# Optimization experiments

Hardware: AMD Instinct MI355X
Metric: run time of the kernel (lower is better)

Reference implementation:

```python
import jax, jax.numpy as jnp
import numpy as np

B, DIM, F, H = 16384, 64, 8, 8
D2 = DIM // 2


def setup_inputs() -> dict:
    key = jax.random.key(0)
    ks = jax.random.split(key, 8)
    s = 0.1  # small init so exp(s_net) stays well-conditioned
    return {
        "x": jax.random.normal(ks[0], (B, DIM), jnp.float32),
        "x_star": jax.random.normal(ks[1], (B, DIM), jnp.float32),
        "W0": jax.random.normal(ks[2], (F, 4, H, D2), jnp.float32) * s,
        "b0": jax.random.normal(ks[3], (F, 4, H), jnp.float32) * s,
        "W1": jax.random.normal(ks[4], (F, 4, H, H), jnp.float32) * s,
        "b1": jax.random.normal(ks[5], (F, 4, H), jnp.float32) * s,
        "W2": jax.random.normal(ks[6], (F, 4, D2, H), jnp.float32) * s,
        "b2": jax.random.normal(ks[7], (F, 4, D2), jnp.float32) * s,
    }


def _fcnn(v, w0, c0, w1, c1, w2, c2):
    # FCNN: Linear -> Tanh -> Linear -> Tanh -> Linear, on a single vector v [D2]
    h = jnp.tanh(w0 @ v + c0)
    h = jnp.tanh(w1 @ h + c1)
    return w2 @ h + c2


def _phi(v, params):
    # Chain of n_flows RealNVP coupling layers on a single sample v [DIM].
    def step(v, p):
        W0, b0, W1, b1, W2, b2 = p  # leading axis 4 = (t1, s1, t2, s2)
        lo, up = v[:D2], v[D2:]
        t1 = _fcnn(lo, W0[0], b0[0], W1[0], b1[0], W2[0], b2[0])
        s1 = _fcnn(lo, W0[1], b0[1], W1[1], b1[1], W2[1], b2[1])
        up = t1 + up * jnp.exp(s1)
        t2 = _fcnn(up, W0[2], b0[2], W1[2], b1[2], W2[2], b2[2])
        s2 = _fcnn(up, W0[3], b0[3], W1[3], b1[3], W2[3], b2[3])
        lo = t2 + lo * jnp.exp(s2)
        return jnp.concatenate([lo, up]), None

    z, _ = jax.lax.scan(step, v, params)
    return z


def reference(x, x_star, W0, b0, W1, b1, W2, b2):
    params = (W0, b0, W1, b1, W2, b2)
    # Per-sample Jacobian of the flow (replaces torch autograd loop): [B, DIM, DIM]
    jac = jax.vmap(jax.jacfwd(lambda v: _phi(v, params)))(x)
    # -grad of quadratic potential (feature=None): -2 * (x - x_star)
    g = -2.0 * (x - x_star)
    # torch.solve(potential_grad, phi_jac): solve J u = g per sample
    return jnp.linalg.solve(jac, g[..., None])[..., 0]
```

## Files before the change

### kernel.cpp

```cpp
#include <hip/hip_runtime.h>


namespace {

typedef __fp16 f16x2 __attribute__((ext_vector_type(2)));
typedef __fp16 v4h __attribute__((ext_vector_type(4)));
typedef __fp16 v8h __attribute__((ext_vector_type(8)));
typedef float f32x4 __attribute__((ext_vector_type(4)));
typedef unsigned int u32;
typedef u32 u32x2 __attribute__((ext_vector_type(2)));
typedef u32 u32x4 __attribute__((ext_vector_type(4)));

constexpr int NB = 16384;

__device__ __forceinline__ float frcp(float x) { return __builtin_amdgcn_rcpf(x); }
__device__ __forceinline__ float ftanh(float x) {
  float e = __expf(2.f * x);
  return 1.f - 2.f * frcp(e + 1.f);
}
__device__ __forceinline__ f16x2 pk(float a, float b) {
  return __builtin_amdgcn_cvt_pkrtz(a, b);
}
__device__ __forceinline__ v8h mk8(f16x2 a, f16x2 b, f16x2 c, f16x2 d) {
  const u32x4 t = {__builtin_bit_cast(u32, a), __builtin_bit_cast(u32, b),
                   __builtin_bit_cast(u32, c), __builtin_bit_cast(u32, d)};
  return __builtin_bit_cast(v8h, t);
}
__device__ __forceinline__ v4h mk4(f16x2 a, f16x2 b) {
  const u32x2 t = {__builtin_bit_cast(u32, a), __builtin_bit_cast(u32, b)};
  return __builtin_bit_cast(v4h, t);
}

__device__ __forceinline__ int pbase(int p) {
  return ((p >> 1) << 2) + ((p & 1) << 1);
}

}

#define L3_FWD(P, BB, D0, D1, D2, D3)                                         \
  do {                                                                        \
    const bool act_ = ((BB) < 2) == (q < 2);                                  \
    v4h Ab = *(const v4h*)(LW2 + ((P)*256 + (BB)*64 + abbase));               \
    Ab = act_ ? Ab : z4;                                                      \
    const f32x4 cb = *(const f32x4*)(LB2 + ((P)*4 + (BB)) * 16 + q * 4);      \
    const f32x4 ob =                                                          \
        __builtin_amdgcn_mfma_f32_16x16x16f16(Ab, H2v, cb, 0, 0, 0);          \
    D0 = ob[0]; D1 = ob[1]; D2 = ob[2]; D3 = ob[3];                           \
  } while (0)

#define FWD_UPD(J, W) W##J = fmaf(W##J, __expf(s##J), t##J)

#define FWD_HALF(P, V, W)                                                     \
  do {                                                                        \
    const v8h Bq = mk8(pk(V##0, V##1), pk(V##2, V##3), pk(V##4, V##5),        \
                       pk(V##6, V##7));                                       \
    const v8h A0 = *(const v8h*)(LW0 + (((P)*64 + q * 16 + n) << 2));         \
    const f32x4 c0 = *(const f32x4*)(LB0 + (P)*16 + q * 4);                   \
    f32x4 d1 = __builtin_amdgcn_mfma_f32_16x16x32_f16(A0, Bq, c0, 0, 0, 0);   \
    const f16x2 H1a = pk(ftanh(d1[0]), ftanh(d1[1]));                         \
    const f16x2 H1b = pk(ftanh(d1[2]), ftanh(d1[3]));                         \
    v4h A1 = *(const v4h*)(LW1 + ((P)*64 + a1off));                           \
    A1 = act1 ? A1 : z4;                                                      \
    const f32x4 c1 = *(const f32x4*)(LB1 + (P)*16 + q * 4);                   \
    f32x4 d2 =                                                                \
        __builtin_amdgcn_mfma_f32_16x16x16f16(A1, mk4(H1a, H1b), c1, 0, 0, 0);\
    const f16x2 H2a = pk(ftanh(d2[0]), ftanh(d2[1]));                         \
    const f16x2 H2b = pk(ftanh(d2[2]), ftanh(d2[3]));                         \
    const v4h H2v = mk4(H2a, H2b);                                            \
    float t0, t1, t2, t3, t4, t5, t6, t7;                                     \
    float s0, s1, s2, s3, s4, s5, s6, s7;                                     \
    L3_FWD(P, 0, t0, t1, t2, t3);                                             \
    L3_FWD(P, 1, t4, t5, t6, t7);                                             \
    L3_FWD(P, 2, s0, s1, s2, s3);                                             \
    L3_FWD(P, 3, s4, s5, s6, s7);                                             \
    FWD_UPD(0, W); FWD_UPD(1, W); FWD_UPD(2, W); FWD_UPD(3, W);               \
    FWD_UPD(4, W); FWD_UPD(5, W); FWD_UPD(6, W); FWD_UPD(7, W);               \
  } while (0)

#define L3_BWD(P, BB, D0, D1, D2, D3, J0, J1, J2, J3)                         \
  do {                                                                        \
    const bool act_ = ((BB) < 2) == (q < 2);                                  \
    v4h Ab = *(const v4h*)(LW2 + ((P)*256 + (BB)*64 + abbase));               \
    Ab = act_ ? Ab : z4;                                                      \
    const f32x4 cb = *(const f32x4*)(LB2 + ((P)*4 + (BB)) * 16 + q * 4);      \
    const f32x4 ob =                                                          \
        __builtin_amdgcn_mfma_f32_16x16x16f16(Ab, H2v, cb, 0, 0, 0);          \
    const f32x4 jb =                                                          \
        __builtin_amdgcn_mfma_f32_16x16x16f16(Ab, G2v, zc, 0, 0, 0);          \
    D0 = ob[0]; D1 = ob[1]; D2 = ob[2]; D3 = ob[3];                           \
    J0 = jb[0]; J1 = jb[1]; J2 = jb[2]; J3 = jb[3];                           \
  } while (0)

#define BWD_INV(J, ST, DME)                                                   \
  do {                                                                        \
    const float esi_ = __expf(-s##J);                                         \
    const float dd_ = ST##J - t##J;                                           \
    ST##J = dd_ * esi_;                                                       \
    DME##J = (DME##J - ut##J - dd_ * us##J) * esi_;                           \
  } while (0)

#define BWD_HALF(P, ST, DME, DOT, VIN)                                        \
  do {                                                                        \
    const v8h Bv = mk8(pk(VIN##0, VIN##1), pk(VIN##2, VIN##3),                \
                       pk(VIN##4, VIN##5), pk(VIN##6, VIN##7));               \
    const v8h Bu = mk8(pk(DOT##0, DOT##1), pk(DOT##2, DOT##3),                \
                       pk(DOT##4, DOT##5), pk(DOT##6, DOT##7));               \
    const v8h A0 = *(const v8h*)(LW0 + (((P)*64 + q * 16 + n) << 2));         \
    const f32x4 c0 = *(const f32x4*)(LB0 + (P)*16 + q * 4);                   \
    f32x4 d1 = __builtin_amdgcn_mfma_f32_16x16x32_f16(A0, Bv, c0, 0, 0, 0);   \
    f32x4 d1u = __builtin_amdgcn_mfma_f32_16x16x32_f16(A0, Bu, zc, 0, 0, 0);  \
    const float h10 = ftanh(d1[0]), h11 = ftanh(d1[1]);                       \
    const float h12 = ftanh(d1[2]), h13 = ftanh(d1[3]);                       \
    const f16x2 H1a = pk(h10, h11);                                           \
    const f16x2 H1b = pk(h12, h13);                                           \
    const f16x2 G1a =                                                         \
        pk((1.f - h10 * h10) * d1u[0], (1.f - h11 * h11) * d1u[1]);           \
    const f16x2 G1b =                                                         \
        pk((1.f - h12 * h12) * d1u[2], (1.f - h13 * h13) * d1u[3]);           \
    v4h A1 = *(const v4h*)(LW1 + ((P)*64 + a1off));                           \
    A1 = act1 ? A1 : z4;                                                      \
    const f32x4 c1 = *(const f32x4*)(LB1 + (P)*16 + q * 4);                   \
    f32x4 d2 =                                                                \
        __builtin_amdgcn_mfma_f32_16x16x16f16(A1, mk4(H1a, H1b), c1, 0, 0, 0);\
    f32x4 d2u =                                                               \
        __builtin_amdgcn_mfma_f32_16x16x16f16(A1, mk4(G1a, G1b), zc, 0, 0, 0);\
    const float h20 = ftanh(d2[0]), h21 = ftanh(d2[1]);                       \
    const float h22 = ftanh(d2[2]), h23 = ftanh(d2[3]);                       \
    const f16x2 G2a =                                                         \
        pk((1.f - h20 * h20) * d2u[0], (1.f - h21 * h21) * d2u[1]);           \
    const f16x2 G2b =                                                         \
        pk((1.f - h22 * h22) * d2u[2], (1.f - h23 * h23) * d2u[3]);           \
    const v4h H2v = mk4(pk(h20, h21), pk(h22, h23));                          \
    const v4h G2v = mk4(G2a, G2b);                                            \
    float t0, t1, t2, t3, t4, t5, t6, t7;                                     \
    float s0, s1, s2, s3, s4, s5, s6, s7;                                     \
    float ut0, ut1, ut2, ut3, ut4, ut5, ut6, ut7;                             \
    float us0, us1, us2, us3, us4, us5, us6, us7;                             \
    L3_BWD(P, 0, t0, t1, t2, t3, ut0, ut1, ut2, ut3);                         \
    L3_BWD(P, 1, t4, t5, t6, t7, ut4, ut5, ut6, ut7);                         \
    L3_BWD(P, 2, s0, s1, s2, s3, us0, us1, us2, us3);                         \
    L3_BWD(P, 3, s4, s5, s6, s7, us4, us5, us6, us7);                         \
    BWD_INV(0, ST, DME); BWD_INV(1, ST, DME);                                 \
    BWD_INV(2, ST, DME); BWD_INV(3, ST, DME);                                 \
    BWD_INV(4, ST, DME); BWD_INV(5, ST, DME);                                 \
    BWD_INV(6, ST, DME); BWD_INV(7, ST, DME);                                 \
  } while (0)

__global__ __attribute__((amdgpu_flat_work_group_size(512, 512),
                          amdgpu_waves_per_eu(4, 8))) void nf_policy_kernel(
    const float* __restrict__ x, const float* __restrict__ xs,
    const float* __restrict__ gW0, const float* __restrict__ gb0,
    const float* __restrict__ gW1, const float* __restrict__ gb1,
    const float* __restrict__ gW2, const float* __restrict__ gb2,
    float* __restrict__ out) {
  __shared__ __align__(16) f16x2 LW0[4096];
  __shared__ __align__(16) f16x2 LW1[1024];
  __shared__ __align__(16) f16x2 LW2[4096];
  __shared__ __align__(16) float LB0[256];
  __shared__ __align__(16) float LB1[256];
  __shared__ __align__(16) float LB2[1024];

  const int tid = threadIdx.x;
  for (int i = tid; i < 4096; i += 512) {
    const int p = i >> 8, rem = i & 255, qq = rem >> 6, rem2 = rem & 63;
    const int mm = rem2 >> 2, w = rem2 & 3;
    const int net = pbase(p) + (mm >> 3);
    const int h = mm & 7, k0 = qq * 8 + w * 2;
    const float* src = gW0 + net * 256 + h * 32 + k0;
    LW0[i] = pk(src[0], src[1]);
  }
  for (int i = tid; i < 1024; i += 512) {
    const int p = i >> 6, rem = i & 63, half = rem >> 5;
    const int row = (rem >> 2) & 7, kk = rem & 3;
    const int net = pbase(p) + half;
    const float* src = gW1 + net * 64 + row * 8 + kk * 2;
    LW1[i] = pk(src[0], src[1]);
  }
  for (int i = tid; i < 4096; i += 512) {
    const int p = i >> 8, rem = i & 255, b = rem >> 6, rem2 = rem & 63;
    const int mm = rem2 >> 2, kk = rem2 & 3;
    const int net = pbase(p) + (b >> 1);
    const int d = 8 * (mm >> 2) + ((b & 1) << 2) + (mm & 3);
    const float* src = gW2 + net * 256 + d * 8 + kk * 2;
    LW2[i] = pk(src[0], src[1]);
  }
  for (int i = tid; i < 256; i += 512) {
    const int p = i >> 4, mm = i & 15;
    const int net = pbase(p) + (mm >> 3);
    LB0[i] = gb0[net * 8 + (mm & 7)];
    LB1[i] = gb1[net * 8 + (mm & 7)];
  }
  for (int i = tid; i < 1024; i += 512) {
    const int p = i >> 6, b = (i >> 4) & 3, mm = i & 15;
    const int net = pbase(p) + (b >> 1);
    const int d = 8 * (mm >> 2) + ((b & 1) << 2) + (mm & 3);
    LB2[i] = gb2[net * 32 + d];
  }
  __syncthreads();

  const int lane = tid & 63;
  const int wv = tid >> 6;
  const int n = lane & 15;
  const int q = lane >> 4;
  const int e = blockIdx.x * 32 + wv * 4 + (n & 3);

  const v4h z4 = {(__fp16)0.f, (__fp16)0.f, (__fp16)0.f, (__fp16)0.f};
  const f32x4 zc = {0.f, 0.f, 0.f, 0.f};
  const bool act1 = (n < 8) == (q < 2);
  const int a1off = ((n & 7) << 2) + ((q & 1) << 1) + ((n >= 8) ? 32 : 0);
  const int abbase = n * 4 + ((q & 1) << 1);

  float lo0, lo1, lo2, lo3, lo4, lo5, lo6, lo7;
  float up0, up1, up2, up3, up4, up5, up6, up7;
  float av0, av1, av2, av3, av4, av5, av6, av7;
  float bv0, bv1, bv2, bv3, bv4, bv5, bv6, bv7;
  {
    const float* xe = x + (size_t)e * 64;
    const float* se = xs + (size_t)e * 64;
    const float4 a0 = *(const float4*)(xe + q * 8);
    const float4 a1 = *(const float4*)(xe + q * 8 + 4);
    const float4 u0 = *(const float4*)(xe + 32 + q * 8);
    const float4 u1 = *(const float4*)(xe + 32 + q * 8 + 4);
    const float4 p0 = *(const float4*)(se + q * 8);
    const float4 p1 = *(const float4*)(se + q * 8 + 4);
    const float4 r0 = *(const float4*)(se + 32 + q * 8);
    const float4 r1 = *(const float4*)(se + 32 + q * 8 + 4);
    lo0 = a0.x; lo1 = a0.y; lo2 = a0.z; lo3 = a0.w;
    lo4 = a1.x; lo5 = a1.y; lo6 = a1.z; lo7 = a1.w;
    up0 = u0.x; up1 = u0.y; up2 = u0.z; up3 = u0.w;
    up4 = u1.x; up5 = u1.y; up6 = u1.z; up7 = u1.w;
    av0 = -2.f * (a0.x - p0.x); av1 = -2.f * (a0.y - p0.y);
    av2 = -2.f * (a0.z - p0.z); av3 = -2.f * (a0.w - p0.w);
    av4 = -2.f * (a1.x - p1.x); av5 = -2.f * (a1.y - p1.y);
    av6 = -2.f * (a1.z - p1.z); av7 = -2.f * (a1.w - p1.w);
    bv0 = -2.f * (u0.x - r0.x); bv1 = -2.f * (u0.y - r0.y);
    bv2 = -2.f * (u0.z - r0.z); bv3 = -2.f * (u0.w - r0.w);
    bv4 = -2.f * (u1.x - r1.x); bv5 = -2.f * (u1.y - r1.y);
    bv6 = -2.f * (u1.z - r1.z); bv7 = -2.f * (u1.w - r1.w);
  }

#pragma clang loop unroll(disable)
  for (int st = 0; st < 8; ++st) {
    const int p0i = 2 * st;
    FWD_HALF(p0i, lo, up);
    FWD_HALF(p0i + 1, up, lo);
  }

#pragma clang loop unroll(disable)
  for (int st = 7; st >= 0; --st) {
    const int p0i = 2 * st;
    BWD_HALF(p0i + 1, lo, av, bv, up);
    BWD_HALF(p0i, up, bv, av, lo);
  }

  if (n < 4) {
    float* oe = out + (size_t)e * 64;
    float4 v;
    v.x = av0; v.y = av1; v.z = av2; v.w = av3;
    *(float4*)(oe + q * 8) = v;
    v.x = av4; v.y = av5; v.z = av6; v.w = av7;
    *(float4*)(oe + q * 8 + 4) = v;
    v.x = bv0; v.y = bv1; v.z = bv2; v.w = bv3;
    *(float4*)(oe + 32 + q * 8) = v;
    v.x = bv4; v.y = bv5; v.z = bv6; v.w = bv7;
    *(float4*)(oe + 32 + q * 8 + 4) = v;
  }
}

extern "C" void kernel_launch(void* const* d_in, const int* in_sizes, int n_in,
                              void* d_out, int out_size, void* d_ws,
                              size_t ws_size, hipStream_t stream) {
  const float* x  = (const float*)d_in[0];
  const float* xs = (const float*)d_in[1];
  const float* W0 = (const float*)d_in[2];
  const float* b0 = (const float*)d_in[3];
  const float* W1 = (const float*)d_in[4];
  const float* b1 = (const float*)d_in[5];
  const float* W2 = (const float*)d_in[6];
  const float* b2 = (const float*)d_in[7];
  float* out = (float*)d_out;

  dim3 grid(NB / 32);
  dim3 block(512);
  nf_policy_kernel<<<grid, block, 0, stream>>>(x, xs, W0, b0, W1, b1, W2, b2,
                                               out);
}
```

Measured before the change: 108.8 us.

## Give each MFMA column its own sample and interleave two sample groups per wave

Before, each wave handled only 4 samples, with each sample copied across 4 MFMA column groups (n&3), so most of the MFMA N dimension held duplicate work. Now each of the 16 columns carries a distinct sample, and each wave processes two 16-sample groups (a and b), whose independent MFMAs are interleaved to hide latency. Blocks shrink to 128 threads covering 64 samples, with waves_per_eu lowered to 1-2 to make room for the doubled register state. Redundant compute drops by roughly 4x per sample, but register pressure rises and occupancy falls, with some risk of spills.

```diff
diff --git a/kernel.cpp b/kernel.cpp
--- a/kernel.cpp
+++ b/kernel.cpp
@@ -37,117 +37,160 @@
 
 }
 
-#define L3_FWD(P, BB, D0, D1, D2, D3)                                         \
+#define MFMA32(A, B, C) __builtin_amdgcn_mfma_f32_16x16x32_f16(A, B, C, 0, 0, 0)
+#define MFMA16(A, B, C) __builtin_amdgcn_mfma_f32_16x16x16f16(A, B, C, 0, 0, 0)
+
+#define L3_FWD2(P, BB, DA0, DA1, DA2, DA3, DB0, DB1, DB2, DB3)                \
   do {                                                                        \
     const bool act_ = ((BB) < 2) == (q < 2);                                  \
     v4h Ab = *(const v4h*)(LW2 + ((P)*256 + (BB)*64 + abbase));               \
     Ab = act_ ? Ab : z4;                                                      \
     const f32x4 cb = *(const f32x4*)(LB2 + ((P)*4 + (BB)) * 16 + q * 4);      \
-    const f32x4 ob =                                                          \
-        __builtin_amdgcn_mfma_f32_16x16x16f16(Ab, H2v, cb, 0, 0, 0);          \
-    D0 = ob[0]; D1 = ob[1]; D2 = ob[2]; D3 = ob[3];                           \
-  } while (0)
-
-#define FWD_UPD(J, W) W##J = fmaf(W##J, __expf(s##J), t##J)
-
-#define FWD_HALF(P, V, W)                                                     \
-  do {                                                                        \
-    const v8h Bq = mk8(pk(V##0, V##1), pk(V##2, V##3), pk(V##4, V##5),        \
-                       pk(V##6, V##7));                                       \
+    const f32x4 oa = MFMA16(Ab, H2va, cb);                                    \
+    const f32x4 ob = MFMA16(Ab, H2vb, cb);                                    \
+    DA0 = oa[0]; DA1 = oa[1]; DA2 = oa[2]; DA3 = oa[3];                       \
+    DB0 = ob[0]; DB1 = ob[1]; DB2 = ob[2]; DB3 = ob[3];                       \
+  } while (0)
+
+#define FWD_UPD(S, J, W) W##S##J = fmaf(W##S##J, __expf(s##S##J), t##S##J)
+
+#define FWD_HALF2(P, V, W)                                                    \
+  do {                                                                        \
+    const v8h Bqa = mk8(pk(V##a0, V##a1), pk(V##a2, V##a3),                   \
+                        pk(V##a4, V##a5), pk(V##a6, V##a7));                  \
+    const v8h Bqb = mk8(pk(V##b0, V##b1), pk(V##b2, V##b3),                   \
+                        pk(V##b4, V##b5), pk(V##b6, V##b7));                  \
     const v8h A0 = *(const v8h*)(LW0 + (((P)*64 + q * 16 + n) << 2));         \
     const f32x4 c0 = *(const f32x4*)(LB0 + (P)*16 + q * 4);                   \
-    f32x4 d1 = __builtin_amdgcn_mfma_f32_16x16x32_f16(A0, Bq, c0, 0, 0, 0);   \
-    const f16x2 H1a = pk(ftanh(d1[0]), ftanh(d1[1]));                         \
-    const f16x2 H1b = pk(ftanh(d1[2]), ftanh(d1[3]));                         \
+    f32x4 d1a = MFMA32(A0, Bqa, c0);                                          \
+    f32x4 d1b = MFMA32(A0, Bqb, c0);                                          \
+    const f16x2 H1aa = pk(ftanh(d1a[0]), ftanh(d1a[1]));                      \
+    const f16x2 H1ab = pk(ftanh(d1a[2]), ftanh(d1a[3]));                      \
+    const f16x2 H1ba = pk(ftanh(d1b[0]), ftanh(d1b[1]));                      \
+    const f16x2 H1bb = pk(ftanh(d1b[2]), ftanh(d1b[3]));                      \
     v4h A1 = *(const v4h*)(LW1 + ((P)*64 + a1off));                           \
     A1 = act1 ? A1 : z4;                                                      \
     const f32x4 c1 = *(const f32x4*)(LB1 + (P)*16 + q * 4);                   \
-    f32x4 d2 =                                                                \
-        __builtin_amdgcn_mfma_f32_16x16x16f16(A1, mk4(H1a, H1b), c1, 0, 0, 0);\
-    const f16x2 H2a = pk(ftanh(d2[0]), ftanh(d2[1]));                         \
-    const f16x2 H2b = pk(ftanh(d2[2]), ftanh(d2[3]));                         \
-    const v4h H2v = mk4(H2a, H2b);                                            \
-    float t0, t1, t2, t3, t4, t5, t6, t7;                                     \
-    float s0, s1, s2, s3, s4, s5, s6, s7;                                     \
-    L3_FWD(P, 0, t0, t1, t2, t3);                                             \
-    L3_FWD(P, 1, t4, t5, t6, t7);                                             \
-    L3_FWD(P, 2, s0, s1, s2, s3);                                             \
-    L3_FWD(P, 3, s4, s5, s6, s7);                                             \
-    FWD_UPD(0, W); FWD_UPD(1, W); FWD_UPD(2, W); FWD_UPD(3, W);               \
-    FWD_UPD(4, W); FWD_UPD(5, W); FWD_UPD(6, W); FWD_UPD(7, W);               \
-  } while (0)
-
-#define L3_BWD(P, BB, D0, D1, D2, D3, J0, J1, J2, J3)                         \
+    f32x4 d2a = MFMA16(A1, mk4(H1aa, H1ab), c1);                              \
+    f32x4 d2b = MFMA16(A1, mk4(H1ba, H1bb), c1);                              \
+    const v4h H2va = mk4(pk(ftanh(d2a[0]), ftanh(d2a[1])),                    \
+                         pk(ftanh(d2a[2]), ftanh(d2a[3])));                   \
+    const v4h H2vb = mk4(pk(ftanh(d2b[0]), ftanh(d2b[1])),                    \
+                         pk(ftanh(d2b[2]), ftanh(d2b[3])));                   \
+    float ta0, ta1, ta2, ta3, ta4, ta5, ta6, ta7;                             \
+    float sa0, sa1, sa2, sa3, sa4, sa5, sa6, sa7;                             \
+    float tb0, tb1, tb2, tb3, tb4, tb5, tb6, tb7;                             \
+    float sb0, sb1, sb2, sb3, sb4, sb5, sb6, sb7;                             \
+    L3_FWD2(P, 0, ta0, ta1, ta2, ta3, tb0, tb1, tb2, tb3);                    \
+    L3_FWD2(P, 1, ta4, ta5, ta6, ta7, tb4, tb5, tb6, tb7);                    \
+    L3_FWD2(P, 2, sa0, sa1, sa2, sa3, sb0, sb1, sb2, sb3);                    \
+    L3_FWD2(P, 3, sa4, sa5, sa6, sa7, sb4, sb5, sb6, sb7);                    \
+    FWD_UPD(a, 0, W); FWD_UPD(a, 1, W); FWD_UPD(a, 2, W); FWD_UPD(a, 3, W);   \
+    FWD_UPD(a, 4, W); FWD_UPD(a, 5, W); FWD_UPD(a, 6, W); FWD_UPD(a, 7, W);   \
+    FWD_UPD(b, 0, W); FWD_UPD(b, 1, W); FWD_UPD(b, 2, W); FWD_UPD(b, 3, W);   \
+    FWD_UPD(b, 4, W); FWD_UPD(b, 5, W); FWD_UPD(b, 6, W); FWD_UPD(b, 7, W);   \
+  } while (0)
+
+#define L3_BWD2(P, BB, DA0, DA1, DA2, DA3, JA0, JA1, JA2, JA3,                \
+                DB0, DB1, DB2, DB3, JB0, JB1, JB2, JB3)                       \
   do {                                                                        \
     const bool act_ = ((BB) < 2) == (q < 2);                                  \
     v4h Ab = *(const v4h*)(LW2 + ((P)*256 + (BB)*64 + abbase));               \
     Ab = act_ ? Ab : z4;                                                      \
     const f32x4 cb = *(const f32x4*)(LB2 + ((P)*4 + (BB)) * 16 + q * 4);      \
-    const f32x4 ob =                                                          \
-        __builtin_amdgcn_mfma_f32_16x16x16f16(Ab, H2v, cb, 0, 0, 0);          \
-    const f32x4 jb =                                                          \
-        __builtin_amdgcn_mfma_f32_16x16x16f16(Ab, G2v, zc, 0, 0, 0);          \
-    D0 = ob[0]; D1 = ob[1]; D2 = ob[2]; D3 = ob[3];                           \
-    J0 = jb[0]; J1 = jb[1]; J2 = jb[2]; J3 = jb[3];                           \
-  } while (0)
-
-#define BWD_INV(J, ST, DME)                                                   \
-  do {                                                                        \
-    const float esi_ = __expf(-s##J);                                         \
-    const float dd_ = ST##J - t##J;                                           \
-    ST##J = dd_ * esi_;                                                       \
-    DME##J = (DME##J - ut##J - dd_ * us##J) * esi_;                           \
-  } while (0)
-
-#define BWD_HALF(P, ST, DME, DOT, VIN)                                        \
-  do {                                                                        \
-    const v8h Bv = mk8(pk(VIN##0, VIN##1), pk(VIN##2, VIN##3),                \
-                       pk(VIN##4, VIN##5), pk(VIN##6, VIN##7));               \
-    const v8h Bu = mk8(pk(DOT##0, DOT##1), pk(DOT##2, DOT##3),                \
-                       pk(DOT##4, DOT##5), pk(DOT##6, DOT##7));               \
+    const f32x4 oa = MFMA16(Ab, H2va, cb);                                    \
+    const f32x4 ja = MFMA16(Ab, G2va, zc);                                    \
+    const f32x4 ob = MFMA16(Ab, H2vb, cb);                                    \
+    const f32x4 jb = MFMA16(Ab, G2vb, zc);                                    \
+    DA0 = oa[0]; DA1 = oa[1]; DA2 = oa[2]; DA3 = oa[3];                       \
+    JA0 = ja[0]; JA1 = ja[1]; JA2 = ja[2]; JA3 = ja[3];                       \
+    DB0 = ob[0]; DB1 = ob[1]; DB2 = ob[2]; DB3 = ob[3];                       \
+    JB0 = jb[0]; JB1 = jb[1]; JB2 = jb[2]; JB3 = jb[3];                       \
+  } while (0)
+
+#define BWD_INV(S, J, ST, DME)                                                \
+  do {                                                                        \
+    const float esi_ = __expf(-s##S##J);                                      \
+    const float dd_ = ST##S##J - t##S##J;                                     \
+    ST##S##J = dd_ * esi_;                                                    \
+    DME##S##J = (DME##S##J - ut##S##J - dd_ * us##S##J) * esi_;               \
+  } while (0)
+
+#define BWD_HALF2(P, ST, DME, DOT, VIN)                                       \
+  do {                                                                        \
+    const v8h Bva = mk8(pk(VIN##a0, VIN##a1), pk(VIN##a2, VIN##a3),           \
+                        pk(VIN##a4, VIN##a5), pk(VIN##a6, VIN##a7));          \
+    const v8h Bua = mk8(pk(DOT##a0, DOT##a1), pk(DOT##a2, DOT##a3),           \
+                        pk(DOT##a4, DOT##a5), pk(DOT##a6, DOT##a7));          \
+    const v8h Bvb = mk8(pk(VIN##b0, VIN##b1), pk(VIN##b2, VIN##b3),           \
+                        pk(VIN##b4, VIN##b5), pk(VIN##b6, VIN##b7));          \
+    const v8h Bub = mk8(pk(DOT##b0, DOT##b1), pk(DOT##b2, DOT##b3),           \
+                        pk(DOT##b4, DOT##b5), pk(DOT##b6, DOT##b7));          \
     const v8h A0 = *(const v8h*)(LW0 + (((P)*64 + q * 16 + n) << 2));         \
     const f32x4 c0 = *(const f32x4*)(LB0 + (P)*16 + q * 4);                   \
-    f32x4 d1 = __builtin_amdgcn_mfma_f32_16x16x32_f16(A0, Bv, c0, 0, 0, 0);   \
-    f32x4 d1u = __builtin_amdgcn_mfma_f32_16x16x32_f16(A0, Bu, zc, 0, 0, 0);  \
-    const float h10 = ftanh(d1[0]), h11 = ftanh(d1[1]);                       \
-    const float h12 = ftanh(d1[2]), h13 = ftanh(d1[3]);                       \
-    const f16x2 H1a = pk(h10, h11);                                           \
-    const f16x2 H1b = pk(h12, h13);                                           \
-    const f16x2 G1a =                                                         \
-        pk((1.f - h10 * h10) * d1u[0], (1.f - h11 * h11) * d1u[1]);           \
-    const f16x2 G1b =                                                         \
-        pk((1.f - h12 * h12) * d1u[2], (1.f - h13 * h13) * d1u[3]);           \
+    f32x4 d1a = MFMA32(A0, Bva, c0);                                          \
+    f32x4 d1ua = MFMA32(A0, Bua, zc);                                         \
+    f32x4 d1b = MFMA32(A0, Bvb, c0);                                          \
+    f32x4 d1ub = MFMA32(A0, Bub, zc);                                         \
+    const float h10a = ftanh(d1a[0]), h11a = ftanh(d1a[1]);                   \
+    const float h12a = ftanh(d1a[2]), h13a = ftanh(d1a[3]);                   \
+    const float h10b = ftanh(d1b[0]), h11b = ftanh(d1b[1]);                   \
+    const float h12b = ftanh(d1b[2]), h13b = ftanh(d1b[3]);                   \
+    const f16x2 G1aa =                                                        \
+        pk((1.f - h10a * h10a) * d1ua[0], (1.f - h11a * h11a) * d1ua[1]);     \
+    const f16x2 G1ab =                                                        \
+        pk((1.f - h12a * h12a) * d1ua[2], (1.f - h13a * h13a) * d1ua[3]);     \
+    const f16x2 G1ba =                                                        \
+        pk((1.f - h10b * h10b) * d1ub[0], (1.f - h11b * h11b) * d1ub[1]);     \
+    const f16x2 G1bb =                                                        \
+        pk((1.f - h12b * h12b) * d1ub[2], (1.f - h13b * h13b) * d1ub[3]);     \
     v4h A1 = *(const v4h*)(LW1 + ((P)*64 + a1off));                           \
     A1 = act1 ? A1 : z4;                                                      \
     const f32x4 c1 = *(const f32x4*)(LB1 + (P)*16 + q * 4);                   \
-    f32x4 d2 =                                                                \
-        __builtin_amdgcn_mfma_f32_16x16x16f16(A1, mk4(H1a, H1b), c1, 0, 0, 0);\
-    f32x4 d2u =                                                               \
-        __builtin_amdgcn_mfma_f32_16x16x16f16(A1, mk4(G1a, G1b), zc, 0, 0, 0);\
-    const float h20 = ftanh(d2[0]), h21 = ftanh(d2[1]);                       \
-    const float h22 = ftanh(d2[2]), h23 = ftanh(d2[3]);                       \
-    const f16x2 G2a =                                                         \
-        pk((1.f - h20 * h20) * d2u[0], (1.f - h21 * h21) * d2u[1]);           \
-    const f16x2 G2b =                                                         \
-        pk((1.f - h22 * h22) * d2u[2], (1.f - h23 * h23) * d2u[3]);           \
-    const v4h H2v = mk4(pk(h20, h21), pk(h22, h23));                          \
-    const v4h G2v = mk4(G2a, G2b);                                            \
-    float t0, t1, t2, t3, t4, t5, t6, t7;                                     \
-    float s0, s1, s2, s3, s4, s5, s6, s7;                                     \
-    float ut0, ut1, ut2, ut3, ut4, ut5, ut6, ut7;                             \
-    float us0, us1, us2, us3, us4, us5, us6, us7;                             \
-    L3_BWD(P, 0, t0, t1, t2, t3, ut0, ut1, ut2, ut3);                         \
-    L3_BWD(P, 1, t4, t5, t6, t7, ut4, ut5, ut6, ut7);                         \
-    L3_BWD(P, 2, s0, s1, s2, s3, us0, us1, us2, us3);                         \
-    L3_BWD(P, 3, s4, s5, s6, s7, us4, us5, us6, us7);                         \
-    BWD_INV(0, ST, DME); BWD_INV(1, ST, DME);                                 \
-    BWD_INV(2, ST, DME); BWD_INV(3, ST, DME);                                 \
-    BWD_INV(4, ST, DME); BWD_INV(5, ST, DME);                                 \
-    BWD_INV(6, ST, DME); BWD_INV(7, ST, DME);                                 \
-  } while (0)
-
-__global__ __attribute__((amdgpu_flat_work_group_size(512, 512),
-                          amdgpu_waves_per_eu(4, 8))) void nf_policy_kernel(
+    f32x4 d2a = MFMA16(A1, mk4(pk(h10a, h11a), pk(h12a, h13a)), c1);          \
+    f32x4 d2ua = MFMA16(A1, mk4(G1aa, G1ab), zc);                             \
+    f32x4 d2b = MFMA16(A1, mk4(pk(h10b, h11b), pk(h12b, h13b)), c1);          \
+    f32x4 d2ub = MFMA16(A1, mk4(G1ba, G1bb), zc);                             \
+    const float h20a = ftanh(d2a[0]), h21a = ftanh(d2a[1]);                   \
+    const float h22a = ftanh(d2a[2]), h23a = ftanh(d2a[3]);                   \
+    const float h20b = ftanh(d2b[0]), h21b = ftanh(d2b[1]);                   \
+    const float h22b = ftanh(d2b[2]), h23b = ftanh(d2b[3]);                   \
+    const v4h H2va = mk4(pk(h20a, h21a), pk(h22a, h23a));                     \
+    const v4h H2vb = mk4(pk(h20b, h21b), pk(h22b, h23b));                     \
+    const v4h G2va =                                                          \
+        mk4(pk((1.f - h20a * h20a) * d2ua[0], (1.f - h21a * h21a) * d2ua[1]), \
+            pk((1.f - h22a * h22a) * d2ua[2], (1.f - h23a * h23a) * d2ua[3]));\
+    const v4h G2vb =                                                          \
+        mk4(pk((1.f - h20b * h20b) * d2ub[0], (1.f - h21b * h21b) * d2ub[1]), \
+            pk((1.f - h22b * h22b) * d2ub[2], (1.f - h23b * h23b) * d2ub[3]));\
+    float ta0, ta1, ta2, ta3, ta4, ta5, ta6, ta7;                             \
+    float sa0, sa1, sa2, sa3, sa4, sa5, sa6, sa7;                             \
+    float uta0, uta1, uta2, uta3, uta4, uta5, uta6, uta7;                     \
+    float usa0, usa1, usa2, usa3, usa4, usa5, usa6, usa7;                     \
+    float tb0, tb1, tb2, tb3, tb4, tb5, tb6, tb7;                             \
+    float sb0, sb1, sb2, sb3, sb4, sb5, sb6, sb7;                             \
+    float utb0, utb1, utb2, utb3, utb4, utb5, utb6, utb7;                     \
+    float usb0, usb1, usb2, usb3, usb4, usb5, usb6, usb7;                     \
+    L3_BWD2(P, 0, ta0, ta1, ta2, ta3, uta0, uta1, uta2, uta3,                 \
+            tb0, tb1, tb2, tb3, utb0, utb1, utb2, utb3);                      \
+    L3_BWD2(P, 1, ta4, ta5, ta6, ta7, uta4, uta5, uta6, uta7,                 \
+            tb4, tb5, tb6, tb7, utb4, utb5, utb6, utb7);                      \
+    L3_BWD2(P, 2, sa0, sa1, sa2, sa3, usa0, usa1, usa2, usa3,                 \
+            sb0, sb1, sb2, sb3, usb0, usb1, usb2, usb3);                      \
+    L3_BWD2(P, 3, sa4, sa5, sa6, sa7, usa4, usa5, usa6, usa7,                 \
+            sb4, sb5, sb6, sb7, usb4, usb5, usb6, usb7);                      \
+    BWD_INV(a, 0, ST, DME); BWD_INV(a, 1, ST, DME);                           \
+    BWD_INV(a, 2, ST, DME); BWD_INV(a, 3, ST, DME);                           \
+    BWD_INV(a, 4, ST, DME); BWD_INV(a, 5, ST, DME);                           \
+    BWD_INV(a, 6, ST, DME); BWD_INV(a, 7, ST, DME);                           \
+    BWD_INV(b, 0, ST, DME); BWD_INV(b, 1, ST, DME);                           \
+    BWD_INV(b, 2, ST, DME); BWD_INV(b, 3, ST, DME);                           \
+    BWD_INV(b, 4, ST, DME); BWD_INV(b, 5, ST, DME);                           \
+    BWD_INV(b, 6, ST, DME); BWD_INV(b, 7, ST, DME);                           \
+  } while (0)
+
+__global__ __attribute__((amdgpu_flat_work_group_size(128, 128),
+                          amdgpu_waves_per_eu(1, 2))) void nf_policy_kernel(
     const float* __restrict__ x, const float* __restrict__ xs,
     const float* __restrict__ gW0, const float* __restrict__ gb0,
     const float* __restrict__ gW1, const float* __restrict__ gb1,
@@ -161,7 +204,7 @@
   __shared__ __align__(16) float LB2[1024];
 
   const int tid = threadIdx.x;
-  for (int i = tid; i < 4096; i += 512) {
+  for (int i = tid; i < 4096; i += 128) {
     const int p = i >> 8, rem = i & 255, qq = rem >> 6, rem2 = rem & 63;
     const int mm = rem2 >> 2, w = rem2 & 3;
     const int net = pbase(p) + (mm >> 3);
@@ -169,14 +212,14 @@
     const float* src = gW0 + net * 256 + h * 32 + k0;
     LW0[i] = pk(src[0], src[1]);
   }
-  for (int i = tid; i < 1024; i += 512) {
+  for (int i = tid; i < 1024; i += 128) {
     const int p = i >> 6, rem = i & 63, half = rem >> 5;
     const int row = (rem >> 2) & 7, kk = rem & 3;
     const int net = pbase(p) + half;
     const float* src = gW1 + net * 64 + row * 8 + kk * 2;
     LW1[i] = pk(src[0], src[1]);
   }
-  for (int i = tid; i < 4096; i += 512) {
+  for (int i = tid; i < 4096; i += 128) {
     const int p = i >> 8, rem = i & 255, b = rem >> 6, rem2 = rem & 63;
     const int mm = rem2 >> 2, kk = rem2 & 3;
     const int net = pbase(p) + (b >> 1);
@@ -184,13 +227,13 @@
     const float* src = gW2 + net * 256 + d * 8 + kk * 2;
     LW2[i] = pk(src[0], src[1]);
   }
-  for (int i = tid; i < 256; i += 512) {
+  for (int i = tid; i < 256; i += 128) {
     const int p = i >> 4, mm = i & 15;
     const int net = pbase(p) + (mm >> 3);
     LB0[i] = gb0[net * 8 + (mm & 7)];
     LB1[i] = gb1[net * 8 + (mm & 7)];
   }
-  for (int i = tid; i < 1024; i += 512) {
+  for (int i = tid; i < 1024; i += 128) {
     const int p = i >> 6, b = (i >> 4) & 3, mm = i & 15;
     const int net = pbase(p) + (b >> 1);
     const int d = 8 * (mm >> 2) + ((b & 1) << 2) + (mm & 3);
@@ -202,7 +245,8 @@
   const int wv = tid >> 6;
   const int n = lane & 15;
   const int q = lane >> 4;
-  const int e = blockIdx.x * 32 + wv * 4 + (n & 3);
+  const int eA = blockIdx.x * 64 + wv * 32 + n;
+  const int eB = eA + 16;
 
   const v4h z4 = {(__fp16)0.f, (__fp16)0.f, (__fp16)0.f, (__fp16)0.f};
   const f32x4 zc = {0.f, 0.f, 0.f, 0.f};
@@ -210,13 +254,17 @@
   const int a1off = ((n & 7) << 2) + ((q & 1) << 1) + ((n >= 8) ? 32 : 0);
   const int abbase = n * 4 + ((q & 1) << 1);
 
-  float lo0, lo1, lo2, lo3, lo4, lo5, lo6, lo7;
-  float up0, up1, up2, up3, up4, up5, up6, up7;
-  float av0, av1, av2, av3, av4, av5, av6, av7;
-  float bv0, bv1, bv2, bv3, bv4, bv5, bv6, bv7;
+  float loa0, loa1, loa2, loa3, loa4, loa5, loa6, loa7;
+  float upa0, upa1, upa2, upa3, upa4, upa5, upa6, upa7;
+  float ava0, ava1, ava2, ava3, ava4, ava5, ava6, ava7;
+  float bva0, bva1, bva2, bva3, bva4, bva5, bva6, bva7;
+  float lob0, lob1, lob2, lob3, lob4, lob5, lob6, lob7;
+  float upb0, upb1, upb2, upb3, upb4, upb5, upb6, upb7;
+  float avb0, avb1, avb2, avb3, avb4, avb5, avb6, avb7;
+  float bvb0, bvb1, bvb2, bvb3, bvb4, bvb5, bvb6, bvb7;
   {
-    const float* xe = x + (size_t)e * 64;
-    const float* se = xs + (size_t)e * 64;
+    const float* xe = x + (size_t)eA * 64;
+    const float* se = xs + (size_t)eA * 64;
     const float4 a0 = *(const float4*)(xe + q * 8);
     const float4 a1 = *(const float4*)(xe + q * 8 + 4);
     const float4 u0 = *(const float4*)(xe + 32 + q * 8);
@@ -225,44 +273,80 @@
     const float4 p1 = *(const float4*)(se + q * 8 + 4);
     const float4 r0 = *(const float4*)(se + 32 + q * 8);
     const float4 r1 = *(const float4*)(se + 32 + q * 8 + 4);
-    lo0 = a0.x; lo1 = a0.y; lo2 = a0.z; lo3 = a0.w;
-    lo4 = a1.x; lo5 = a1.y; lo6 = a1.z; lo7 = a1.w;
-    up0 = u0.x; up1 = u0.y; up2 = u0.z; up3 = u0.w;
-    up4 = u1.x; up5 = u1.y; up6 = u1.z; up7 = u1.w;
-    av0 = -2.f * (a0.x - p0.x); av1 = -2.f * (a0.y - p0.y);
-    av2 = -2.f * (a0.z - p0.z); av3 = -2.f * (a0.w - p0.w);
-    av4 = -2.f * (a1.x - p1.x); av5 = -2.f * (a1.y - p1.y);
-    av6 = -2.f * (a1.z - p1.z); av7 = -2.f * (a1.w - p1.w);
-    bv0 = -2.f * (u0.x - r0.x); bv1 = -2.f * (u0.y - r0.y);
-    bv2 = -2.f * (u0.z - r0.z); bv3 = -2.f * (u0.w - r0.w);
-    bv4 = -2.f * (u1.x - r1.x); bv5 = -2.f * (u1.y - r1.y);
-    bv6 = -2.f * (u1.z - r1.z); bv7 = -2.f * (u1.w - r1.w);
+    loa0 = a0.x; loa1 = a0.y; loa2 = a0.z; loa3 = a0.w;
+    loa4 = a1.x; loa5 = a1.y; loa6 = a1.z; loa7 = a1.w;
+    upa0 = u0.x; upa1 = u0.y; upa2 = u0.z; upa3 = u0.w;
+    upa4 = u1.x; upa5 = u1.y; upa6 = u1.z; upa7 = u1.w;
+    ava0 = -2.f * (a0.x - p0.x); ava1 = -2.f * (a0.y - p0.y);
+    ava2 = -2.f * (a0.z - p0.z); ava3 = -2.f * (a0.w - p0.w);
+    ava4 = -2.f * (a1.x - p1.x); ava5 = -2.f * (a1.y - p1.y);
+    ava6 = -2.f * (a1.z - p1.z); ava7 = -2.f * (a1.w - p1.w);
+    bva0 = -2.f * (u0.x - r0.x); bva1 = -2.f * (u0.y - r0.y);
+    bva2 = -2.f * (u0.z - r0.z); bva3 = -2.f * (u0.w - r0.w);
+    bva4 = -2.f * (u1.x - r1.x); bva5 = -2.f * (u1.y - r1.y);
+    bva6 = -2.f * (u1.z - r1.z); bva7 = -2.f * (u1.w - r1.w);
+  }
+  {
+    const float* xe = x + (size_t)eB * 64;
+    const float* se = xs + (size_t)eB * 64;
+    const float4 a0 = *(const float4*)(xe + q * 8);
+    const float4 a1 = *(const float4*)(xe + q * 8 + 4);
+    const float4 u0 = *(const float4*)(xe + 32 + q * 8);
+    const float4 u1 = *(const float4*)(xe + 32 + q * 8 + 4);
+    const float4 p0 = *(const float4*)(se + q * 8);
+    const float4 p1 = *(const float4*)(se + q * 8 + 4);
+    const float4 r0 = *(const float4*)(se + 32 + q * 8);
+    const float4 r1 = *(const float4*)(se + 32 + q * 8 + 4);
+    lob0 = a0.x; lob1 = a0.y; lob2 = a0.z; lob3 = a0.w;
+    lob4 = a1.x; lob5 = a1.y; lob6 = a1.z; lob7 = a1.w;
+    upb0 = u0.x; upb1 = u0.y; upb2 = u0.z; upb3 = u0.w;
+    upb4 = u1.x; upb5 = u1.y; upb6 = u1.z; upb7 = u1.w;
+    avb0 = -2.f * (a0.x - p0.x); avb1 = -2.f * (a0.y - p0.y);
+    avb2 = -2.f * (a0.z - p0.z); avb3 = -2.f * (a0.w - p0.w);
+    avb4 = -2.f * (a1.x - p1.x); avb5 = -2.f * (a1.y - p1.y);
+    avb6 = -2.f * (a1.z - p1.z); avb7 = -2.f * (a1.w - p1.w);
+    bvb0 = -2.f * (u0.x - r0.x); bvb1 = -2.f * (u0.y - r0.y);
+    bvb2 = -2.f * (u0.z - r0.z); bvb3 = -2.f * (u0.w - r0.w);
+    bvb4 = -2.f * (u1.x - r1.x); bvb5 = -2.f * (u1.y - r1.y);
+    bvb6 = -2.f * (u1.z - r1.z); bvb7 = -2.f * (u1.w - r1.w);
   }
 
 #pragma clang loop unroll(disable)
   for (int st = 0; st < 8; ++st) {
     const int p0i = 2 * st;
-    FWD_HALF(p0i, lo, up);
-    FWD_HALF(p0i + 1, up, lo);
+    FWD_HALF2(p0i, lo, up);
+    FWD_HALF2(p0i + 1, up, lo);
   }
 
 #pragma clang loop unroll(disable)
   for (int st = 7; st >= 0; --st) {
     const int p0i = 2 * st;
-    BWD_HALF(p0i + 1, lo, av, bv, up);
-    BWD_HALF(p0i, up, bv, av, lo);
-  }
-
-  if (n < 4) {
-    float* oe = out + (size_t)e * 64;
+    BWD_HALF2(p0i + 1, lo, av, bv, up);
+    BWD_HALF2(p0i, up, bv, av, lo);
+  }
+
+  {
+    float* oe = out + (size_t)eA * 64;
     float4 v;
-    v.x = av0; v.y = av1; v.z = av2; v.w = av3;
+    v.x = ava0; v.y = ava1; v.z = ava2; v.w = ava3;
     *(float4*)(oe + q * 8) = v;
-    v.x = av4; v.y = av5; v.z = av6; v.w = av7;
+    v.x = ava4; v.y = ava5; v.z = ava6; v.w = ava7;
     *(float4*)(oe + q * 8 + 4) = v;
-    v.x = bv0; v.y = bv1; v.z = bv2; v.w = bv3;
+    v.x = bva0; v.y = bva1; v.z = bva2; v.w = bva3;
     *(float4*)(oe + 32 + q * 8) = v;
-    v.x = bv4; v.y = bv5; v.z = bv6; v.w = bv7;
+    v.x = bva4; v.y = bva5; v.z = bva6; v.w = bva7;
+    *(float4*)(oe + 32 + q * 8 + 4) = v;
+  }
+  {
+    float* oe = out + (size_t)eB * 64;
+    float4 v;
+    v.x = avb0; v.y = avb1; v.z = avb2; v.w = avb3;
+    *(float4*)(oe + q * 8) = v;
+    v.x = avb4; v.y = avb5; v.z = avb6; v.w = avb7;
+    *(float4*)(oe + q * 8 + 4) = v;
+    v.x = bvb0; v.y = bvb1; v.z = bvb2; v.w = bvb3;
+    *(float4*)(oe + 32 + q * 8) = v;
+    v.x = bvb4; v.y = bvb5; v.z = bvb6; v.w = bvb7;
     *(float4*)(oe + 32 + q * 8 + 4) = v;
   }
 }
@@ -280,8 +364,8 @@
   const float* b2 = (const float*)d_in[7];
   float* out = (float*)d_out;
 
-  dim3 grid(NB / 32);
-  dim3 block(512);
+  dim3 grid(NB / 64);
+  dim3 block(128);
   nf_policy_kernel<<<grid, block, 0, stream>>>(x, xs, W0, b0, W1, b1, W2, b2,
                                                out);
 }
```

Result: slower. 113.3 us (+4.2%).
